# Optimization experiments

Hardware: AMD Instinct MI355X
Metric: run time of the kernel (lower is better)

## Reference

```python
import jax, jax.numpy as jnp
import numpy as np

B, N, E, H = 4, 2048, 288, 8
D = E // H  # head_dim = 36


def setup_inputs() -> dict:
    key = jax.random.key(0)
    ks = jax.random.split(key, 8)
    s = 1.0 / np.sqrt(E)
    return {
        "query": jax.random.normal(ks[0], (B, N, E), jnp.float32),
        "key": jax.random.normal(ks[1], (B, N, E), jnp.float32),
        "value": jax.random.normal(ks[2], (B, N, E), jnp.float32),
        "Wq": jax.random.normal(ks[3], (E, E), jnp.float32) * s,
        "bq": jnp.zeros((E,), jnp.float32),
        "Wk": jax.random.normal(ks[4], (E, E), jnp.float32) * s,
        "bk": jnp.zeros((E,), jnp.float32),
        "Wv": jax.random.normal(ks[5], (E, E), jnp.float32) * s,
        "bv": jnp.zeros((E,), jnp.float32),
        "Wo": jax.random.normal(ks[6], (E, E), jnp.float32) * s,
        "bo": jnp.zeros((E,), jnp.float32),
    }


def reference(query, key, value, Wq, bq, Wk, bk, Wv, bv, Wo, bo):
    scaling = float(D) ** (-0.5)
    q = (query @ Wq + bq) * scaling            # (B, N, E), pre-scaled as in source
    k = key @ Wk + bk                          # (B, N, E)
    v = value @ Wv + bv                        # (B, N, E)
    # split heads: per-head slices along last dim == reshape to (B, N, H, D)
    qh = q.reshape(B, N, H, D)
    kh = k.reshape(B, N, H, D)
    vh = v.reshape(B, N, H, D)
    scores = jnp.einsum("bnhd,bmhd->bhnm", qh, kh)   # (B, H, N, N)
    attn = jax.nn.softmax(scores, axis=-1)
    out = jnp.einsum("bhnm,bmhd->bnhd", attn, vh)    # (B, N, H, D)
    out = out.reshape(B, N, E)                       # concat heads
    return out @ Wo + bo
```

## Files before the change

### kernel.cpp

```cpp
#include <hip/hip_runtime.h>

#define E 288
#define NSEQ 2048
#define BATCH 4
#define NH 8
#define HD 36
#define BH (BATCH * NH)
#define ROWS (BATCH * NSEQ)
#define BHN (BH * NSEQ)

typedef _Float16 half8_t __attribute__((ext_vector_type(8)));
typedef _Float16 half4_t __attribute__((ext_vector_type(4)));
typedef _Float16 half2_t __attribute__((ext_vector_type(2)));
typedef float f32x4 __attribute__((ext_vector_type(4)));
typedef int i32x4 __attribute__((ext_vector_type(4)));

__device__ __forceinline__ int sw64(int row, int col) {
  return (row << 6) + ((((col >> 3) ^ row) & 7) << 3) + (col & 7);
}

__device__ __forceinline__ int toff(int r, int k) {
  const int rp = r >> 1;
  const int g = (((r & 1) << 2) + (k >> 3)) ^ (rp & 7);
  return (rp << 6) + ((g & 7) << 3) + (k & 7);
}

__device__ __forceinline__ void gld16(const _Float16* g, _Float16* l) {
  __builtin_amdgcn_global_load_lds(
      (const __attribute__((address_space(1))) void*)g,
      (__attribute__((address_space(3))) void*)l, 16, 0, 0);
}

__device__ __forceinline__ float fexp2(float x) {
  return __builtin_amdgcn_exp2f(x);
}

__device__ __forceinline__ unsigned pack_h2(float a, float b) {
  union { half2_t h; unsigned u; } cv;
  cv.h[0] = (_Float16)a;
  cv.h[1] = (_Float16)b;
  return cv.u;
}

__device__ __forceinline__ void plswap16(unsigned& a, unsigned& b) {
  asm("v_permlane16_swap_b32 %0, %1" : "+v"(a), "+v"(b));
}
__device__ __forceinline__ void plswap32(unsigned& a, unsigned& b) {
  asm("v_permlane32_swap_b32 %0, %1" : "+v"(a), "+v"(b));
}

#define WBLK 1296
#define QZBLK 2048

__global__ __launch_bounds__(256) void prep_kernel(
    const float* __restrict__ Wq, const float* __restrict__ Wk,
    const float* __restrict__ Wv, const float* __restrict__ Wo,
    _Float16* __restrict__ wblk, _Float16* __restrict__ q16) {
  const int bid = blockIdx.x;
  const int tid = threadIdx.x;
  if (bid < WBLK) {
    const int j = bid * 256 + tid;
    const int m = j / (E * E);
    const int rem = j - m * (E * E);
    const int k = rem / E, n = rem - k * E;
    const float* W = (m == 0) ? Wq : (m == 1) ? Wk : (m == 2) ? Wv : Wo;
    wblk[(size_t)((m * 3 + n / 96) * 9 + (k >> 5)) * 3072 +
         toff(n % 96, k & 31)] = (_Float16)W[(size_t)k * E + n];
  } else {
    const int j = (bid - WBLK) * 256 + tid;
    ((i32x4*)q16)[j] = (i32x4){0, 0, 0, 0};
  }
}

#define PM 128
#define PN 96

struct QKVArgs {
  const float* x[3];
  const float* bias[3];
  _Float16* out[3];
};

__global__ __launch_bounds__(256, 4) void proj_qkv_kernel(
    QKVArgs A, const _Float16* __restrict__ wblk) {
  __shared__ __align__(16) _Float16 abuf[2][4096];
  __shared__ __align__(16) _Float16 wbuf[2][3072];

  const int tid = threadIdx.x;
  const int lane = tid & 63, w = tid >> 6;
  const int quad = lane >> 4, l15 = lane & 15;
  const int mode = blockIdx.z;
  const int RB = blockIdx.x, CT = blockIdx.y;
  const float* __restrict__ x = A.x[mode];
  const _Float16* __restrict__ wb = wblk + (size_t)(mode * 3 + CT) * 9 * 3072;
  const int row0 = RB * PM;

  float4 apre[4];
  auto loadA = [&](int C) {
#pragma unroll
    for (int iu = 0; iu < 4; ++iu) {
      const int i = tid + 256 * iu, r = i >> 3, c4 = i & 7;
      apre[iu] = *(const float4*)&x[(size_t)(row0 + r) * E + C * 32 + c4 * 4];
    }
  };
  auto writeA = [&](_Float16* dst) {
#pragma unroll
    for (int iu = 0; iu < 4; ++iu) {
      const int i = tid + 256 * iu, r = i >> 3, c4 = i & 7;
      half4_t h = {(_Float16)apre[iu].x, (_Float16)apre[iu].y,
                   (_Float16)apre[iu].z, (_Float16)apre[iu].w};
      *(half4_t*)&dst[toff(r, c4 * 4)] = h;
    }
  };

  f32x4 acc[2][6];
#pragma unroll
  for (int t = 0; t < 2; ++t)
#pragma unroll
    for (int nt = 0; nt < 6; ++nt) acc[t][nt] = (f32x4){0.f, 0.f, 0.f, 0.f};

  loadA(0);
  writeA(abuf[0]);
  for (int seg = w; seg < 6; seg += 4)
    gld16(wb + seg * 512 + lane * 8, wbuf[0] + seg * 512);
  loadA(1);

  for (int C = 0; C < 9; ++C) {
    const int cur = C & 1;
    __syncthreads();
    if (C + 1 < 9) {
      for (int seg = w; seg < 6; seg += 4)
        gld16(wb + (C + 1) * 3072 + seg * 512 + lane * 8,
              wbuf[cur ^ 1] + seg * 512);
      writeA(abuf[cur ^ 1]);
      if (C + 2 < 9) loadA(C + 2);
    }
    half8_t ah[2];
#pragma unroll
    for (int t = 0; t < 2; ++t)
      ah[t] = *(const half8_t*)&abuf[cur][toff(w * 32 + t * 16 + l15, quad * 8)];
#pragma unroll
    for (int nt = 0; nt < 6; ++nt) {
      const half8_t bf = *(const half8_t*)&wbuf[cur][toff(nt * 16 + l15, quad * 8)];
#pragma unroll
      for (int t = 0; t < 2; ++t)
        acc[t][nt] = __builtin_amdgcn_mfma_f32_16x16x32_f16(ah[t], bf, acc[t][nt], 0, 0, 0);
    }
  }

  const float* __restrict__ bias = A.bias[mode];
  _Float16* __restrict__ outp = A.out[mode];
  const float scale = (mode == 0) ? 0.24044917348149868f : 1.0f;
  const int col0 = CT * PN;
#pragma unroll
  for (int nt = 0; nt < 6; ++nt) {
    const int col = col0 + nt * 16 + l15;
    const int h = col / 36, d = col - h * 36;
    const float bc = bias[col];
#pragma unroll
    for (int t = 0; t < 2; ++t) {
#pragma unroll
      for (int r = 0; r < 4; ++r) {
        const int row = row0 + w * 32 + t * 16 + quad * 4 + r;
        const int b = row >> 11, n = row & (NSEQ - 1);
        const int bh = b * NH + h;
        const _Float16 val = (_Float16)((acc[t][nt][r] + bc) * scale);
        if (mode == 0) {
          outp[((size_t)bh * NSEQ + n) * 64 + d] = val;
        } else {
          const int kt = n >> 6, c = n & 63;
          if (mode == 1) {
            outp[((size_t)bh * 32 + kt) * 4096 + sw64(c, d)] = val;
          } else {
            const int pc = ((c & 15) << 2) | (c >> 4);
            outp[((size_t)bh * 32 + kt) * 3072 + sw64(d, pc)] = val;
          }
        }
      }
    }
  }
}

#define QB 128
#define KT 64
#define SPLIT 4

__device__ __forceinline__ void stage_tile(const _Float16* kg, const _Float16* vg,
                                           _Float16* kb, _Float16* vb, int w,
                                           int lane) {
#pragma unroll
  for (int seg = w; seg < 8; seg += 4)
    gld16(kg + seg * 512 + lane * 8, kb + seg * 512);
  for (int seg = w; seg < 6; seg += 4)
    gld16(vg + seg * 512 + lane * 8, vb + seg * 512);
}

__global__ __launch_bounds__(256, 4) void attn_kernel(
    const _Float16* __restrict__ q16, const _Float16* __restrict__ kblk,
    const _Float16* __restrict__ vblk, _Float16* __restrict__ pacc16,
    float* __restrict__ psum) {
  __shared__ __align__(16) _Float16 kbuf[2][KT * 64];
  __shared__ __align__(16) _Float16 vbuf[2][48 * 64];

  const int tid = threadIdx.x;
  const int lane = tid & 63;
  const int w = tid >> 6;
  const int quad = lane >> 4;
  const int l15 = lane & 15;

  const int id = blockIdx.x;
  const int xcd = id & 7;
  const int qb = (id >> 3) & 15;
  const int g = id >> 7;
  const int bhc = g * 8 + xcd;
  const int bh = bhc >> 2;
  const int chunk = bhc & 3;
  const int q0 = qb * QB;

  const _Float16* qbase = q16 + ((size_t)bh * NSEQ + q0 + w * 32) * 64;
  half8_t qf[2][2];
#pragma unroll
  for (int t = 0; t < 2; ++t)
#pragma unroll
    for (int kc = 0; kc < 2; ++kc)
      qf[t][kc] = *(const half8_t*)&qbase[(t * 16 + l15) * 64 + kc * 32 + quad * 8];

  f32x4 oacc[2][3];
#pragma unroll
  for (int t = 0; t < 2; ++t)
#pragma unroll
    for (int nt = 0; nt < 3; ++nt) oacc[t][nt] = (f32x4){0.f, 0.f, 0.f, 0.f};
  float ssum[2] = {0.f, 0.f};

  const int t0 = chunk * 8;
  const _Float16* kbase = kblk + ((size_t)bh * 32 + t0) * 4096;
  const _Float16* vbase = vblk + ((size_t)bh * 32 + t0) * 3072;

  stage_tile(kbase, vbase, kbuf[0], vbuf[0], w, lane);

  for (int it = 0; it < 8; ++it) {
    const int cur = it & 1;
    __syncthreads();
    if (it + 1 < 8)
      stage_tile(kbase + (it + 1) * 4096, vbase + (it + 1) * 3072,
                 kbuf[cur ^ 1], vbuf[cur ^ 1], w, lane);

    unsigned pk[2][4][2];
#pragma unroll
    for (int a = 0; a < 2; ++a) {
      f32x4 sc[2][2];
#pragma unroll
      for (int sp = 0; sp < 2; ++sp) {
        const int s = a * 2 + sp;
        const half8_t kf0 = *(const half8_t*)&kbuf[cur][sw64(s * 16 + l15, quad * 8)];
        const half8_t kf1 = *(const half8_t*)&kbuf[cur][sw64(s * 16 + l15, 32 + quad * 8)];
#pragma unroll
        for (int t = 0; t < 2; ++t) {
          f32x4 c0 = __builtin_amdgcn_mfma_f32_16x16x32_f16(
              kf0, qf[t][0], (f32x4){0.f, 0.f, 0.f, 0.f}, 0, 0, 0);
          sc[t][sp] = __builtin_amdgcn_mfma_f32_16x16x32_f16(
              kf1, qf[t][1], c0, 0, 0, 0);
        }
      }
#pragma unroll
      for (int t = 0; t < 2; ++t)
#pragma unroll
        for (int r = 0; r < 4; ++r) {
          const float p0 = fexp2(sc[t][0][r]);
          const float p1 = fexp2(sc[t][1][r]);
          ssum[t] += p0 + p1;
          pk[t][r][a] = pack_h2(p0, p1);
        }
    }

    half8_t pa[2][2];
#pragma unroll
    for (int t = 0; t < 2; ++t) {
      union { unsigned u[4]; half8_t h; } f0, f1;
#pragma unroll
      for (int v = 0; v < 4; ++v) {
        unsigned x = pk[t][v >> 1][v & 1];
        unsigned y = pk[t][(v >> 1) + 2][v & 1];
        plswap16(x, y);
        plswap32(x, y);
        f0.u[v] = x;
        f1.u[v] = y;
      }
      pa[t][0] = f0.h;
      pa[t][1] = f1.h;
    }

#pragma unroll
    for (int kc = 0; kc < 2; ++kc)
#pragma unroll
      for (int nt = 0; nt < 3; ++nt) {
        const half8_t vf = *(const half8_t*)&vbuf[cur][sw64(nt * 16 + l15, kc * 32 + quad * 8)];
#pragma unroll
        for (int t = 0; t < 2; ++t)
          oacc[t][nt] = __builtin_amdgcn_mfma_f32_16x16x32_f16(pa[t][kc], vf, oacc[t][nt], 0, 0, 0);
      }
  }

#pragma unroll
  for (int t = 0; t < 2; ++t) {
    float s = ssum[t];
    s += __shfl_xor(s, 16);
    s += __shfl_xor(s, 32);
    const int rowq = q0 + w * 32 + t * 16 + l15;
    const size_t grq = (size_t)chunk * BHN + (size_t)bh * NSEQ + rowq;
    if (lane < 16) psum[grq] = s;
#pragma unroll
    for (int r = 0; r < 4; ++r) {
      const int row = q0 + w * 32 + t * 16 + quad * 4 + r;
      const size_t gr = (size_t)chunk * BHN + (size_t)bh * NSEQ + row;
#pragma unroll
      for (int nt = 0; nt < 3; ++nt) {
        const int col = nt * 16 + l15;
        if (col < HD) pacc16[gr * HD + col] = (_Float16)oacc[t][nt][r];
      }
    }
  }
}

__global__ __launch_bounds__(256) void combine_kernel(
    const _Float16* __restrict__ pacc16, const float* __restrict__ psum,
    _Float16* __restrict__ abh, _Float16* __restrict__ abl) {
  const int idx = blockIdx.x * 256 + threadIdx.x;
  if (idx >= BHN * 9) return;
  const int gr = idx / 9;
  const int d4 = idx - gr * 9;

  float a[4] = {0.f, 0.f, 0.f, 0.f};
  float s = 0.f;
#pragma unroll
  for (int c = 0; c < SPLIT; ++c) {
    const half4_t p = *(const half4_t*)&pacc16[((size_t)c * BHN + gr) * HD + d4 * 4];
#pragma unroll
    for (int j = 0; j < 4; ++j) a[j] += (float)p[j];
    s += psum[(size_t)c * BHN + gr];
  }
  const float inv = 1.0f / s;
  const int bh = gr >> 11;
  const int n = gr & (NSEQ - 1);
  const int b = bh >> 3, h = bh & 7;
  const int row = b * NSEQ + n;
  const int col = h * 36 + d4 * 4;

  half4_t hv, lv;
#pragma unroll
  for (int j = 0; j < 4; ++j) {
    const float val = a[j] * inv;
    const _Float16 hi = (_Float16)val;
    hv[j] = hi;
    lv[j] = (_Float16)(val - (float)hi);
  }
  const size_t o = (size_t)((row >> 6) * 9 + (col >> 5)) * 2048 + toff(row & 63, col & 31);
  *(half4_t*)&abh[o] = hv;
  *(half4_t*)&abl[o] = lv;
}

__global__ __launch_bounds__(256, 4) void proj_o_kernel(
    const _Float16* __restrict__ abh, const _Float16* __restrict__ abl,
    const _Float16* __restrict__ wblk_o, const float* __restrict__ bias,
    float* __restrict__ out) {
  __shared__ __align__(16) _Float16 hbuf[2][2048];
  __shared__ __align__(16) _Float16 lbuf[2][2048];
  __shared__ __align__(16) _Float16 wbuf[2][3072];

  const int tid = threadIdx.x;
  const int lane = tid & 63, w = tid >> 6;
  const int quad = lane >> 4, l15 = lane & 15;
  const int RB = blockIdx.x, CT = blockIdx.y;
  const _Float16* __restrict__ hblk = abh + (size_t)RB * 9 * 2048;
  const _Float16* __restrict__ lblk = abl + (size_t)RB * 9 * 2048;
  const _Float16* __restrict__ wb = wblk_o + (size_t)CT * 9 * 3072;

  f32x4 acc[6];
#pragma unroll
  for (int nt = 0; nt < 6; ++nt) acc[nt] = (f32x4){0.f, 0.f, 0.f, 0.f};

  gld16(hblk + w * 512 + lane * 8, hbuf[0] + w * 512);
  gld16(lblk + w * 512 + lane * 8, lbuf[0] + w * 512);
  for (int seg = w; seg < 6; seg += 4)
    gld16(wb + seg * 512 + lane * 8, wbuf[0] + seg * 512);

  for (int C = 0; C < 9; ++C) {
    const int cur = C & 1;
    __syncthreads();
    if (C + 1 < 9) {
      gld16(hblk + (C + 1) * 2048 + w * 512 + lane * 8, hbuf[cur ^ 1] + w * 512);
      gld16(lblk + (C + 1) * 2048 + w * 512 + lane * 8, lbuf[cur ^ 1] + w * 512);
      for (int seg = w; seg < 6; seg += 4)
        gld16(wb + (C + 1) * 3072 + seg * 512 + lane * 8, wbuf[cur ^ 1] + seg * 512);
    }
    const half8_t ah = *(const half8_t*)&hbuf[cur][toff(w * 16 + l15, quad * 8)];
    const half8_t al = *(const half8_t*)&lbuf[cur][toff(w * 16 + l15, quad * 8)];
#pragma unroll
    for (int nt = 0; nt < 6; ++nt) {
      const half8_t bf = *(const half8_t*)&wbuf[cur][toff(nt * 16 + l15, quad * 8)];
      acc[nt] = __builtin_amdgcn_mfma_f32_16x16x32_f16(ah, bf, acc[nt], 0, 0, 0);
      acc[nt] = __builtin_amdgcn_mfma_f32_16x16x32_f16(al, bf, acc[nt], 0, 0, 0);
    }
  }

#pragma unroll
  for (int nt = 0; nt < 6; ++nt) {
    const int col = CT * PN + nt * 16 + l15;
    const float bc = bias[col];
#pragma unroll
    for (int r = 0; r < 4; ++r) {
      const int row = RB * 64 + w * 16 + quad * 4 + r;
      out[(size_t)row * E + col] = acc[nt][r] + bc;
    }
  }
}

extern "C" void kernel_launch(void* const* d_in, const int* in_sizes, int n_in,
                              void* d_out, int out_size, void* d_ws,
                              size_t ws_size, hipStream_t stream) {
  const float* query = (const float*)d_in[0];
  const float* key_ = (const float*)d_in[1];
  const float* value = (const float*)d_in[2];
  const float* Wq = (const float*)d_in[3];
  const float* bq = (const float*)d_in[4];
  const float* Wk = (const float*)d_in[5];
  const float* bk = (const float*)d_in[6];
  const float* Wv = (const float*)d_in[7];
  const float* bv = (const float*)d_in[8];
  const float* Wo = (const float*)d_in[9];
  const float* bo = (const float*)d_in[10];
  float* out = (float*)d_out;

  _Float16* q16 = (_Float16*)d_ws;
  _Float16* kblk = q16 + (size_t)BH * NSEQ * 64;
  _Float16* vblk = kblk + (size_t)BH * 32 * 4096;
  _Float16* wblk = vblk + (size_t)BH * 32 * 3072;
  _Float16* abh = wblk + (size_t)4 * 3 * 9 * 3072;
  _Float16* abl = abh + (size_t)128 * 9 * 2048;
  _Float16* pacc16 = abl + (size_t)128 * 9 * 2048;
  float* psum = (float*)(pacc16 + (size_t)SPLIT * BHN * HD);

  prep_kernel<<<WBLK + QZBLK, 256, 0, stream>>>(Wq, Wk, Wv, Wo, wblk, q16);

  QKVArgs qa;
  qa.x[0] = query; qa.x[1] = key_; qa.x[2] = value;
  qa.bias[0] = bq; qa.bias[1] = bk; qa.bias[2] = bv;
  qa.out[0] = q16; qa.out[1] = kblk; qa.out[2] = vblk;
  proj_qkv_kernel<<<dim3(ROWS / PM, E / PN, 3), 256, 0, stream>>>(qa, wblk);

  attn_kernel<<<dim3((NSEQ / QB) * BH * SPLIT), 256, 0, stream>>>(
      q16, kblk, vblk, pacc16, psum);

  combine_kernel<<<(BHN * 9) / 256, 256, 0, stream>>>(pacc16, psum, abh, abl);

  proj_o_kernel<<<dim3(ROWS / 64, E / PN), 256, 0, stream>>>(
      abh, abl, wblk + (size_t)3 * 3 * 9 * 3072, bo, out);
}
```

Measured before the change: 162.2 us.

## Fold softmax row sum into PV MFMA via ones column in V padding

Writes a column of ones into the padded V column 36 of every V tile, so the P·V MFMA also produces the softmax denominator. This removes the per-element sum accumulation and the cross-lane shuffle reduction at the end of the kernel. The change also preloads the V fragments before the QK phase, wraps the MFMA blocks in s_setprio, and raises launch bounds to 5 waves per SIMD. Preloading raises register pressure, and the row sum is now taken from fp16-rounded P, which slightly changes precision.

Result: slower. 214.8 us (+32.4%).

```diff
diff --git a/kernel.cpp b/kernel.cpp
--- a/kernel.cpp
+++ b/kernel.cpp
@@ -51,11 +51,13 @@
 
 #define WBLK 1296
 #define QZBLK 2048
+#define VOBLK 256
 
 __global__ __launch_bounds__(256) void prep_kernel(
     const float* __restrict__ Wq, const float* __restrict__ Wk,
     const float* __restrict__ Wv, const float* __restrict__ Wo,
-    _Float16* __restrict__ wblk, _Float16* __restrict__ q16) {
+    _Float16* __restrict__ wblk, _Float16* __restrict__ q16,
+    _Float16* __restrict__ vblk) {
   const int bid = blockIdx.x;
   const int tid = threadIdx.x;
   if (bid < WBLK) {
@@ -66,9 +68,15 @@
     const float* W = (m == 0) ? Wq : (m == 1) ? Wk : (m == 2) ? Wv : Wo;
     wblk[(size_t)((m * 3 + n / 96) * 9 + (k >> 5)) * 3072 +
          toff(n % 96, k & 31)] = (_Float16)W[(size_t)k * E + n];
-  } else {
+  } else if (bid < WBLK + QZBLK) {
     const int j = (bid - WBLK) * 256 + tid;
     ((i32x4*)q16)[j] = (i32x4){0, 0, 0, 0};
+  } else {
+    const int j = (bid - WBLK - QZBLK) * 256 + tid;
+    const int bh = j >> 11;
+    const int rem = j & 2047;
+    const int kt = rem >> 6, c = rem & 63;
+    vblk[((size_t)bh * 32 + kt) * 3072 + sw64(36, c)] = (_Float16)1.0f;
   }
 }
 
@@ -195,7 +203,7 @@
     gld16(vg + seg * 512 + lane * 8, vb + seg * 512);
 }
 
-__global__ __launch_bounds__(256, 4) void attn_kernel(
+__global__ __launch_bounds__(256, 5) void attn_kernel(
     const _Float16* __restrict__ q16, const _Float16* __restrict__ kblk,
     const _Float16* __restrict__ vblk, _Float16* __restrict__ pacc16,
     float* __restrict__ psum) {
@@ -230,7 +238,6 @@
   for (int t = 0; t < 2; ++t)
 #pragma unroll
     for (int nt = 0; nt < 3; ++nt) oacc[t][nt] = (f32x4){0.f, 0.f, 0.f, 0.f};
-  float ssum[2] = {0.f, 0.f};
 
   const int t0 = chunk * 8;
   const _Float16* kbase = kblk + ((size_t)bh * 32 + t0) * 4096;
@@ -245,10 +252,18 @@
       stage_tile(kbase + (it + 1) * 4096, vbase + (it + 1) * 3072,
                  kbuf[cur ^ 1], vbuf[cur ^ 1], w, lane);
 
+    half8_t vf[2][3];
+#pragma unroll
+    for (int kc = 0; kc < 2; ++kc)
+#pragma unroll
+      for (int nt = 0; nt < 3; ++nt)
+        vf[kc][nt] = *(const half8_t*)&vbuf[cur][sw64(nt * 16 + l15, kc * 32 + quad * 8)];
+
     unsigned pk[2][4][2];
 #pragma unroll
     for (int a = 0; a < 2; ++a) {
       f32x4 sc[2][2];
+      __builtin_amdgcn_s_setprio(1);
 #pragma unroll
       for (int sp = 0; sp < 2; ++sp) {
         const int s = a * 2 + sp;
@@ -262,13 +277,13 @@
               kf1, qf[t][1], c0, 0, 0, 0);
         }
       }
+      __builtin_amdgcn_s_setprio(0);
 #pragma unroll
       for (int t = 0; t < 2; ++t)
 #pragma unroll
         for (int r = 0; r < 4; ++r) {
           const float p0 = fexp2(sc[t][0][r]);
           const float p1 = fexp2(sc[t][1][r]);
-          ssum[t] += p0 + p1;
           pk[t][r][a] = pack_h2(p0, p1);
         }
     }
@@ -290,29 +305,25 @@
       pa[t][1] = f1.h;
     }
 
+    __builtin_amdgcn_s_setprio(1);
 #pragma unroll
     for (int kc = 0; kc < 2; ++kc)
 #pragma unroll
       for (int nt = 0; nt < 3; ++nt) {
-        const half8_t vf = *(const half8_t*)&vbuf[cur][sw64(nt * 16 + l15, kc * 32 + quad * 8)];
 #pragma unroll
         for (int t = 0; t < 2; ++t)
-          oacc[t][nt] = __builtin_amdgcn_mfma_f32_16x16x32_f16(pa[t][kc], vf, oacc[t][nt], 0, 0, 0);
+          oacc[t][nt] = __builtin_amdgcn_mfma_f32_16x16x32_f16(pa[t][kc], vf[kc][nt], oacc[t][nt], 0, 0, 0);
       }
+    __builtin_amdgcn_s_setprio(0);
   }
 
 #pragma unroll
   for (int t = 0; t < 2; ++t) {
-    float s = ssum[t];
-    s += __shfl_xor(s, 16);
-    s += __shfl_xor(s, 32);
-    const int rowq = q0 + w * 32 + t * 16 + l15;
-    const size_t grq = (size_t)chunk * BHN + (size_t)bh * NSEQ + rowq;
-    if (lane < 16) psum[grq] = s;
 #pragma unroll
     for (int r = 0; r < 4; ++r) {
       const int row = q0 + w * 32 + t * 16 + quad * 4 + r;
       const size_t gr = (size_t)chunk * BHN + (size_t)bh * NSEQ + row;
+      if (l15 == 4) psum[gr] = oacc[t][2][r];
 #pragma unroll
       for (int nt = 0; nt < 3; ++nt) {
         const int col = nt * 16 + l15;
@@ -440,7 +451,8 @@
   _Float16* pacc16 = abl + (size_t)128 * 9 * 2048;
   float* psum = (float*)(pacc16 + (size_t)SPLIT * BHN * HD);
 
-  prep_kernel<<<WBLK + QZBLK, 256, 0, stream>>>(Wq, Wk, Wv, Wo, wblk, q16);
+  prep_kernel<<<WBLK + QZBLK + VOBLK, 256, 0, stream>>>(Wq, Wk, Wv, Wo, wblk,
+                                                        q16, vblk);
 
   QKVArgs qa;
   qa.x[0] = query; qa.x[1] = key_; qa.x[2] = value;
```
